# Performance work log

Hardware: AMD Instinct MI355X
Metric: run time of the kernel (lower is better)

## Reference

```python
import jax, jax.numpy as jnp
import numpy as np
from jax import lax

STRIDE = (1, 1)
PADDING = ((1, 1), (1, 1))
DILATION = (1, 1)
GROUPS = 1


def setup_inputs() -> dict:
    key = jax.random.key(0)
    k1, k2, k3, k4, k5 = jax.random.split(key, 5)
    # quantized int8-ish activations/weights stored as float (as in the torch module)
    x = jax.random.randint(k1, (32, 128, 56, 56), -128, 128).astype(jnp.float32)
    weight_int = jax.random.randint(k2, (256, 128, 3, 3), -128, 128).astype(jnp.float32)
    bias_int = jax.random.randint(k3, (256,), -1024, 1024).astype(jnp.float32)
    A = jax.random.randint(k4, (256,), 1, 32768)  # per-channel requant multiplier
    N = jax.random.randint(k5, (256,), 16, 25)    # per-channel shift
    return {
        "x": x,
        "weight_int": weight_int,
        "bias_int": bias_int,
        "A": A,
        "N": N,
        "out_min": 0,
        "out_max": 255,
    }


def reference(x, weight_int, bias_int, A, N, out_min, out_max):
    # emulate torch's x.int().float() truncation casts
    xq = jnp.trunc(x)
    wq = jnp.trunc(weight_int)
    bq = jnp.trunc(bias_int)
    out = lax.conv_general_dilated(
        xq, wq,
        window_strides=STRIDE,
        padding=PADDING,
        rhs_dilation=DILATION,
        feature_group_count=GROUPS,
        dimension_numbers=("NCHW", "OIHW", "NCHW"),
    )
    out = jnp.round(out + bq[None, :, None, None])
    # out *= A ; out >>= N  (torch float rshift == divide by 2**N)
    Af = A.astype(jnp.float32)[None, :, None, None]
    Nf = N.astype(jnp.float32)[None, :, None, None]
    out = out * Af / jnp.exp2(Nf)
    if out_min >= 0:
        out = jnp.clip(jnp.round(out), float(out_min), float(out_max))
    return out
```

## Files before the change

kernel.cpp:

```cpp
#include <hip/hip_runtime.h>
#include <stdint.h>

typedef int   v4i __attribute__((ext_vector_type(4)));
typedef float v4f __attribute__((ext_vector_type(4)));

#define XT_H_STRIDE (66*128)
#define XT_N_STRIDE (58*66*128)
#define XT_BYTES    (32*58*66*128)
#define WQ_BYTES    (256*1152)

__device__ __forceinline__ void gload16(const void* g, void* l) {
  __builtin_amdgcn_global_load_lds(
      (const __attribute__((address_space(1))) void*)g,
      (__attribute__((address_space(3))) void*)l, 16, 0, 0);
}

__global__ __launch_bounds__(256) void xform_x(const float* __restrict__ x,
                                               char* __restrict__ xt) {
  __shared__ int LB[56 * 33];
  int bid = blockIdx.x;
  int n  = bid / 58;
  int hp = bid - n * 58;
  int t  = threadIdx.x;
  int srch = hp - 1;
  bool rowok = (srch >= 0) && (srch < 56);
  char* dstrow = xt + (size_t)n * XT_N_STRIDE + (size_t)hp * XT_H_STRIDE;

  if (rowok) {
    const float* rb = x + ((size_t)(n * 128) * 56 + srch) * 56;
#pragma unroll
    for (int u0 = 0; u0 < 2; ++u0) {
      int u  = t + u0 * 256;
      int wb = u & 15;
      int cb = u >> 4;
      int w0 = wb * 4, ci0 = cb * 4;
      if (w0 < 56) {
        int dw[4] = {0, 0, 0, 0};
#pragma unroll
        for (int i = 0; i < 4; ++i) {
          v4f f = *(const v4f*)(rb + (size_t)(ci0 + i) * 3136 + w0);
#pragma unroll
          for (int j = 0; j < 4; ++j)
            dw[j] |= (((int)f[j]) & 255) << (8 * i);
        }
#pragma unroll
        for (int j = 0; j < 4; ++j)
          LB[(w0 + j) * 33 + cb] = dw[j];
      }
    }
    __syncthreads();
    for (int c = t; c < 528; c += 256) {
      int wp  = c >> 3;
      int cio = c & 7;
      int srw = wp - 1;
      v4i v = {0, 0, 0, 0};
      if (srw >= 0 && srw < 56) {
#pragma unroll
        for (int k = 0; k < 4; ++k) v[k] = LB[srw * 33 + cio * 4 + k];
      }
      *(v4i*)(dstrow + c * 16) = v;
    }
  } else {
    v4i z = {0, 0, 0, 0};
    for (int c = t; c < 528; c += 256) *(v4i*)(dstrow + c * 16) = z;
  }
}

__global__ __launch_bounds__(256) void xform_w(const float* __restrict__ wsrc,
                                               const int* __restrict__ Aq,
                                               const int* __restrict__ Nq,
                                               char* __restrict__ wq2,
                                               float* __restrict__ scale) {
  int idx = blockIdx.x * 256 + threadIdx.x;
  int co = idx / 1152;
  int k  = idx - co * 1152;
  int g  = k >> 7;
  int ci = k & 127;
  int kh = g / 3;
  int kw = g - 3 * kh;
  float f = wsrc[(size_t)(co * 128 + ci) * 9 + kh * 3 + kw];
  wq2[((k >> 6) * 256 + co) * 64 + (k & 63)] = (signed char)(int)f;
  if (idx < 256) {
    scale[idx] = (float)Aq[idx] * exp2f(-(float)Nq[idx]);
  }
}

__global__ __launch_bounds__(256, 3) void qconv_gemm(
    const char* __restrict__ xt, const char* __restrict__ wq2,
    const float* __restrict__ bias, const float* __restrict__ scale,
    const int* __restrict__ pmin, const int* __restrict__ pmax,
    float* __restrict__ out) {
  __shared__ __align__(16) char Bp[4 * 8448];

  int bid = blockIdx.x;
  int xcd = bid & 7;
  int q   = bid >> 3;
  int mt  = q & 1;
  int nt  = xcd * 112 + (q >> 1);
  int n   = nt / 28;
  int ht  = nt - n * 28;
  int h0  = ht * 2;
  int m0  = mt * 128;

  int t  = threadIdx.x;
  int wv = t >> 6;
  int ln = t & 63;
  int quad = ln >> 4;
  int l16  = ln & 15;
  int wm = wv & 1, wn = wv >> 1;

  const char* xb = xt + (size_t)n * XT_N_STRIDE + (size_t)h0 * XT_H_STRIDE;
  const char* abase = wq2 + (size_t)(m0 + wm * 64 + l16) * 64 + quad * 16;

  for (int it = 0; it < 9; ++it) {
    int s = t + it * 256;
    if (s < 2112) {
      int row = s / 528;
      int rr  = s - row * 528;
      int w   = rr >> 3;
      int cq  = rr & 7;
      gload16(xb + row * XT_H_STRIDE + w * 128 + ((cq ^ (w & 7)) << 4),
              Bp + it * 4096 + wv * 1024);
    }
  }

  v4i a[4], b[4], an[4], bn[4];
#pragma unroll
  for (int i = 0; i < 4; ++i)
    a[i] = *(const v4i*)(abase + i * 1024);

  asm volatile("s_waitcnt vmcnt(0)" ::: "memory");
  __syncthreads();

  {
    const char* bb = Bp + wn * XT_H_STRIDE + l16 * 128 + ((quad ^ (l16 & 7)) << 4);
#pragma unroll
    for (int j = 0; j < 4; ++j)
      b[j] = *(const v4i*)(bb + j * 2048);
  }

  v4i acc[4][4];
#pragma unroll
  for (int i = 0; i < 4; ++i)
#pragma unroll
    for (int j = 0; j < 4; ++j) {
      v4i z = {0, 0, 0, 0};
      acc[i][j] = z;
    }

#pragma unroll
  for (int kt = 0; kt < 18; ++kt) {
    if (kt < 17) {
      const int kn  = kt + 1;
      const int pn  = kn & 1;
      const int gn  = kn >> 1;
      const int khn = gn / 3;
      const int kwn = gn - 3 * khn;
      const char* ak = abase + (size_t)kn * 16384;
#pragma unroll
      for (int i = 0; i < 4; ++i)
        an[i] = *(const v4i*)(ak + i * 1024);
      int bswzn = (((pn << 2) + quad) ^ ((l16 + kwn) & 7)) << 4;
      const char* bbn = Bp + (wn + khn) * XT_H_STRIDE + (l16 + kwn) * 128 + bswzn;
#pragma unroll
      for (int j = 0; j < 4; ++j)
        bn[j] = *(const v4i*)(bbn + j * 2048);
      __builtin_amdgcn_sched_barrier(0);
      asm volatile("s_waitcnt vmcnt(4) lgkmcnt(4)" ::: "memory");
      __builtin_amdgcn_sched_barrier(0);
    } else {
      __builtin_amdgcn_sched_barrier(0);
      asm volatile("s_waitcnt vmcnt(0) lgkmcnt(0)" ::: "memory");
      __builtin_amdgcn_sched_barrier(0);
    }

    __builtin_amdgcn_s_setprio(1);
#pragma unroll
    for (int i = 0; i < 4; ++i)
#pragma unroll
      for (int j = 0; j < 4; ++j)
        acc[i][j] = __builtin_amdgcn_mfma_i32_16x16x64_i8(a[i], b[j], acc[i][j], 0, 0, 0);
    __builtin_amdgcn_s_setprio(0);

    if (kt < 17) {
#pragma unroll
      for (int u = 0; u < 4; ++u) { a[u] = an[u]; b[u] = bn[u]; }
    }
  }

  float mn = (float)pmin[0];
  float mx = (float)pmax[0];
#pragma unroll
  for (int i = 0; i < 4; ++i) {
    int co_b = m0 + wm * 64 + i * 16 + quad * 4;
#pragma unroll
    for (int r = 0; r < 4; ++r) {
      int co = co_b + r;
      float bs = bias[co];
      float sc = scale[co];
#pragma unroll
      for (int j = 0; j < 4; ++j) {
        int sl = wn * 64 + j * 16 + l16;
        int w  = sl & 63;
        int dh = sl >> 6;
        if (w < 56) {
          float f = (float)acc[i][j][r] + bs;
          f = rintf(f * sc);
          f = fminf(fmaxf(f, mn), mx);
          out[(((size_t)n * 256 + co) * 56 + (h0 + dh)) * 56 + w] = f;
        }
      }
    }
  }
}

extern "C" void kernel_launch(void* const* d_in, const int* in_sizes, int n_in,
                              void* d_out, int out_size, void* d_ws, size_t ws_size,
                              hipStream_t stream) {
  const float* x  = (const float*)d_in[0];
  const float* w  = (const float*)d_in[1];
  const float* b  = (const float*)d_in[2];
  const int*   Aq = (const int*)d_in[3];
  const int*   Nq = (const int*)d_in[4];
  const int*   mn = (const int*)d_in[5];
  const int*   mx = (const int*)d_in[6];
  float* out = (float*)d_out;

  char*  xt    = (char*)d_ws;
  char*  wq2   = xt + XT_BYTES;
  float* scale = (float*)(wq2 + WQ_BYTES);

  hipLaunchKernelGGL(xform_x, dim3(32 * 58), dim3(256), 0, stream, x, xt);
  hipLaunchKernelGGL(xform_w, dim3(1152), dim3(256), 0, stream, w, Aq, Nq, wq2, scale);
  hipLaunchKernelGGL(qconv_gemm, dim3(1792), dim3(256), 0, stream,
                     xt, wq2, b, scale, mn, mx, out);
}
```

Baseline: 193.4 us.

## Stage weight tiles through triple-buffered LDS with async global-to-LDS loads

```diff
diff --git a/kernel.cpp b/kernel.cpp
--- a/kernel.cpp
+++ b/kernel.cpp
@@ -69,7 +69,7 @@
 __global__ __launch_bounds__(256) void xform_w(const float* __restrict__ wsrc,
                                                const int* __restrict__ Aq,
                                                const int* __restrict__ Nq,
-                                               char* __restrict__ wq2,
+                                               char* __restrict__ wq3,
                                                float* __restrict__ scale) {
   int idx = blockIdx.x * 256 + threadIdx.x;
   int co = idx / 1152;
@@ -79,18 +79,24 @@
   int kh = g / 3;
   int kw = g - 3 * kh;
   float f = wsrc[(size_t)(co * 128 + ci) * 9 + kh * 3 + kw];
-  wq2[((k >> 6) * 256 + co) * 64 + (k & 63)] = (signed char)(int)f;
+  int kt    = k >> 6;
+  int mhalf = co >> 7;
+  int chunk = (k >> 4) & 3;
+  int row   = co & 127;
+  int col   = k & 15;
+  wq3[(((kt * 2 + mhalf) * 4 + chunk) * 128 + row) * 16 + col] = (signed char)(int)f;
   if (idx < 256) {
     scale[idx] = (float)Aq[idx] * exp2f(-(float)Nq[idx]);
   }
 }
 
-__global__ __launch_bounds__(256, 3) void qconv_gemm(
-    const char* __restrict__ xt, const char* __restrict__ wq2,
+__global__ __launch_bounds__(256, 2) void qconv_gemm(
+    const char* __restrict__ xt, const char* __restrict__ wq3,
     const float* __restrict__ bias, const float* __restrict__ scale,
     const int* __restrict__ pmin, const int* __restrict__ pmax,
     float* __restrict__ out) {
   __shared__ __align__(16) char Bp[4 * 8448];
+  __shared__ __align__(16) char As[3][8192];
 
   int bid = blockIdx.x;
   int xcd = bid & 7;
@@ -109,8 +115,8 @@
   int l16  = ln & 15;
   int wm = wv & 1, wn = wv >> 1;
 
-  const char* xb = xt + (size_t)n * XT_N_STRIDE + (size_t)h0 * XT_H_STRIDE;
-  const char* abase = wq2 + (size_t)(m0 + wm * 64 + l16) * 64 + quad * 16;
+  const char* xb    = xt + (size_t)n * XT_N_STRIDE + (size_t)h0 * XT_H_STRIDE;
+  const char* wbase = wq3 + mt * 8192;
 
   for (int it = 0; it < 9; ++it) {
     int s = t + it * 256;
@@ -123,15 +129,16 @@
               Bp + it * 4096 + wv * 1024);
     }
   }
-
-  v4i a[4], b[4], an[4], bn[4];
-#pragma unroll
-  for (int i = 0; i < 4; ++i)
-    a[i] = *(const v4i*)(abase + i * 1024);
-
-  asm volatile("s_waitcnt vmcnt(0)" ::: "memory");
-  __syncthreads();
-
+#pragma unroll
+  for (int kk = 0; kk < 2; ++kk) {
+    const char* src = wbase + kk * 16384;
+    gload16(src + t * 16,        As[kk] + wv * 1024);
+    gload16(src + 4096 + t * 16, As[kk] + 4096 + wv * 1024);
+  }
+  asm volatile("s_waitcnt vmcnt(2)" ::: "memory");
+  asm volatile("s_barrier" ::: "memory");
+
+  v4i a[4], b[4], bn[4];
   {
     const char* bb = Bp + wn * XT_H_STRIDE + l16 * 128 + ((quad ^ (l16 & 7)) << 4);
 #pragma unroll
@@ -150,41 +157,54 @@
 
 #pragma unroll
   for (int kt = 0; kt < 18; ++kt) {
+    const int p = kt % 3;
+
+    if (kt < 16) {
+      const char* src = wbase + (kt + 2) * 16384;
+      char* dst = As[(kt + 2) % 3];
+      gload16(src + t * 16,        dst + wv * 1024);
+      gload16(src + 4096 + t * 16, dst + 4096 + wv * 1024);
+    }
+
+    const char* ab = As[p] + quad * 2048 + (wm * 64 + l16) * 16;
+#pragma unroll
+    for (int i = 0; i < 4; ++i)
+      a[i] = *(const v4i*)(ab + i * 256);
+
+    __builtin_amdgcn_sched_barrier(0);
+    asm volatile("s_waitcnt lgkmcnt(0)" ::: "memory");
+    __builtin_amdgcn_sched_barrier(0);
+
+    __builtin_amdgcn_s_setprio(1);
+#pragma unroll
+    for (int i = 0; i < 4; ++i)
+#pragma unroll
+      for (int j = 0; j < 4; ++j)
+        acc[i][j] = __builtin_amdgcn_mfma_i32_16x16x64_i8(a[i], b[j], acc[i][j], 0, 0, 0);
+    __builtin_amdgcn_s_setprio(0);
+
     if (kt < 17) {
       const int kn  = kt + 1;
       const int pn  = kn & 1;
       const int gn  = kn >> 1;
       const int khn = gn / 3;
       const int kwn = gn - 3 * khn;
-      const char* ak = abase + (size_t)kn * 16384;
-#pragma unroll
-      for (int i = 0; i < 4; ++i)
-        an[i] = *(const v4i*)(ak + i * 1024);
       int bswzn = (((pn << 2) + quad) ^ ((l16 + kwn) & 7)) << 4;
       const char* bbn = Bp + (wn + khn) * XT_H_STRIDE + (l16 + kwn) * 128 + bswzn;
 #pragma unroll
       for (int j = 0; j < 4; ++j)
         bn[j] = *(const v4i*)(bbn + j * 2048);
+
       __builtin_amdgcn_sched_barrier(0);
-      asm volatile("s_waitcnt vmcnt(4) lgkmcnt(4)" ::: "memory");
-      __builtin_amdgcn_sched_barrier(0);
-    } else {
-      __builtin_amdgcn_sched_barrier(0);
-      asm volatile("s_waitcnt vmcnt(0) lgkmcnt(0)" ::: "memory");
-      __builtin_amdgcn_sched_barrier(0);
-    }
-
-    __builtin_amdgcn_s_setprio(1);
-#pragma unroll
-    for (int i = 0; i < 4; ++i)
-#pragma unroll
-      for (int j = 0; j < 4; ++j)
-        acc[i][j] = __builtin_amdgcn_mfma_i32_16x16x64_i8(a[i], b[j], acc[i][j], 0, 0, 0);
-    __builtin_amdgcn_s_setprio(0);
-
-    if (kt < 17) {
-#pragma unroll
-      for (int u = 0; u < 4; ++u) { a[u] = an[u]; b[u] = bn[u]; }
+      if (kt < 16) {
+        asm volatile("s_waitcnt vmcnt(2)" ::: "memory");
+      } else {
+        asm volatile("s_waitcnt vmcnt(0)" ::: "memory");
+      }
+      asm volatile("s_barrier" ::: "memory");
+
+#pragma unroll
+      for (int u = 0; u < 4; ++u) b[u] = bn[u];
     }
   }
 
@@ -227,11 +247,11 @@
   float* out = (float*)d_out;
 
   char*  xt    = (char*)d_ws;
-  char*  wq2   = xt + XT_BYTES;
-  float* scale = (float*)(wq2 + WQ_BYTES);
+  char*  wq3   = xt + XT_BYTES;
+  float* scale = (float*)(wq3 + WQ_BYTES);
 
   hipLaunchKernelGGL(xform_x, dim3(32 * 58), dim3(256), 0, stream, x, xt);
-  hipLaunchKernelGGL(xform_w, dim3(1152), dim3(256), 0, stream, w, Aq, Nq, wq2, scale);
+  hipLaunchKernelGGL(xform_w, dim3(1152), dim3(256), 0, stream, w, Aq, Nq, wq3, scale);
   hipLaunchKernelGGL(qconv_gemm, dim3(1792), dim3(256), 0, stream,
-                     xt, wq2, b, scale, mn, mx, out);
-}
+                     xt, wq3, b, scale, mn, mx, out);
+}
```

Measured after the change: 196.1 us. No clear change (+1.4%).
